# Performance work log

Hardware: AMD Instinct MI355X
Metric: run time of the kernel (lower is better)

The kernel has to match this reference:

```python
import jax, jax.numpy as jnp
import numpy as np

LP, LQ, B, D = 4096, 4096, 32, 512  # lp, lq, batch, hidden (=in_size1=in_size2)
WSCALE = 0.04  # ~ torch Linear default uniform bound 1/sqrt(512)


def setup_inputs() -> dict:
    key = jax.random.key(0)
    ks = jax.random.split(key, 11)
    return {
        "h": jax.random.normal(ks[0], (LP, B, D), jnp.float32),
        "u": jax.random.normal(ks[1], (B, LQ, D), jnp.float32),
        "v": jax.random.normal(ks[2], (B, D, 1), jnp.float32),
        "Wu_w": jax.random.normal(ks[3], (D, D), jnp.float32) * WSCALE,
        "Wu_b": jax.random.normal(ks[4], (D,), jnp.float32) * WSCALE,
        "Wh_w": jax.random.normal(ks[5], (D, D), jnp.float32) * WSCALE,
        "Wha_w": jax.random.normal(ks[6], (D, D), jnp.float32) * WSCALE,
        "W_ih": jax.random.normal(ks[7], (3 * D, D), jnp.float32) * WSCALE,
        "W_hh": jax.random.normal(ks[8], (3 * D, D), jnp.float32) * WSCALE,
        "b_ih": jax.random.normal(ks[9], (3 * D,), jnp.float32) * WSCALE,
        "b_hh": jax.random.normal(ks[10], (3 * D,), jnp.float32) * WSCALE,
    }


def _gru_cell(x, hprev, W_ih, W_hh, b_ih, b_hh):
    # torch GRUCell semantics
    gi = x @ W_ih.T + b_ih          # [B, 3D]
    gh = hprev @ W_hh.T + b_hh      # [B, 3D]
    i_r, i_z, i_n = jnp.split(gi, 3, axis=-1)
    h_r, h_z, h_n = jnp.split(gh, 3, axis=-1)
    r = jax.nn.sigmoid(i_r + h_r)
    z = jax.nn.sigmoid(i_z + h_z)
    n = jnp.tanh(i_n + r * h_n)
    return (1.0 - z) * n + z * hprev


def reference(h, u, v, Wu_w, Wu_b, Wh_w, Wha_w, W_ih, W_hh, b_ih, b_hh):
    # h: [lp, B, d1], u: [B, lq, d2], v: [B, H, 1]
    vb = v[:, :, 0]  # [B, H]
    # --- attention over u ---
    xq = jnp.tanh(jnp.einsum('bqd,hd->bqh', u, Wu_w) + Wu_b)   # [B, lq, H]
    s = jnp.einsum('bqh,bh->bq', xq, vb)                        # bmm(x, v).squeeze
    a = jax.nn.softmax(s, axis=1)
    r = jnp.einsum('bq,bqd->bd', a, u)                          # [B, d2]
    # --- attention over h conditioned on r, twice with GRU update in between ---
    Whh_proj = jnp.einsum('pbd,hd->pbh', h, Wh_w)               # [lp, B, H] (reused)

    def h_attn(rvec):
        x = jnp.tanh(Whh_proj + (rvec @ Wha_w.T)[None])         # [lp, B, H]
        s = jnp.einsum('pbh,bh->bp', x, vb)                     # [B, lp]
        return jax.nn.softmax(s, axis=1)

    p1 = h_attn(r)
    c = jnp.einsum('bp,pbd->bd', p1, h)                         # [B, d1]
    r2 = _gru_cell(c, r, W_ih, W_hh, b_ih, b_hh)                # [B, d2]
    p2 = h_attn(r2)
    return (p1, p2)
```

## Files before the change

kernel.cpp:

```cpp
#include <hip/hip_runtime.h>
#include <hip/hip_bf16.h>

typedef __attribute__((ext_vector_type(4))) float f4;
typedef __attribute__((ext_vector_type(8))) _Float16 h8;
typedef __attribute__((ext_vector_type(4))) _Float16 h4;

#define MTOT 131072

__device__ __forceinline__ float fast_tanh(float x){
    float e = exp2f(x * 2.8853900817779268f);
    return 1.0f - 2.0f * __builtin_amdgcn_rcpf(e + 1.0f);
}
__device__ __forceinline__ float fast_sigmoid(float x){
    return __builtin_amdgcn_rcpf(1.0f + exp2f(-x * 1.4426950408889634f));
}
__device__ __forceinline__ float wave_reduce_sum(float v){
    #pragma unroll
    for (int off = 32; off; off >>= 1) v += __shfl_down(v, off, 64);
    return v;
}

__device__ __forceinline__ void gl_lds16(const void* g, void* l){
    __builtin_amdgcn_global_load_lds(
        (const __attribute__((address_space(1))) void*)g,
        (__attribute__((address_space(3))) void*)l, 16, 0, 0);
}

__global__ __launch_bounds__(256) void k_pack_both(
    const float* __restrict__ Wu, const float* __restrict__ Wh,
    _Float16* __restrict__ Pu, _Float16* __restrict__ Ph)
{
    const int g = blockIdx.x;
    const float* W = (g < 128) ? Wu : Wh;
    _Float16*    P = (g < 128) ? Pu : Ph;
    const int idx = (g & 127) * 4 + (threadIdx.x >> 6);
    const int l = threadIdx.x & 63;
    const int n = (idx >> 4) * 16 + (l & 15);
    const int k = (idx & 15) * 32 + (l >> 4) * 8;
    const float* src = W + n * 512 + k;
    f4 s0 = *(const f4*)(src);
    f4 s1 = *(const f4*)(src + 4);
    h8 v;
    #pragma unroll
    for (int i = 0; i < 4; i++){ v[i] = (_Float16)s0[i]; v[4+i] = (_Float16)s1[i]; }
    *(h8*)(P + (idx << 9) + l * 8) = v;
}

union SMem {
    struct { float A[2][4096]; _Float16 W[2][8192]; } st;
    _Float16 ep[64][264];
};

template<int MODE>
__global__ __launch_bounds__(512) void k_score_gemm(
    const float* __restrict__ A,
    const _Float16* __restrict__ Wp,
    const float* __restrict__ vb,
    const float* __restrict__ addvec,
    float* __restrict__ spart,
    _Float16* __restrict__ whh)
{
    __shared__ __align__(16) SMem sm;

    const int tid  = threadIdx.x;
    const int lane = tid & 63;
    const int wv   = tid >> 6;
    const int wr   = wv >> 2;
    const int wc   = wv & 3;
    const int swz  = ((blockIdx.x & 7) << 8) | (blockIdx.x >> 3);
    const int mt   = swz >> 1;
    const int nc   = swz & 1;
    const int m0   = mt * 128;
    const int n0   = nc * 256;

    const int lr = lane & 15;
    const int kq = lane >> 4;

    const int arow0 = tid >> 3;
    const int aseg  = tid & 7;

    auto stage = [&](int kt, int buf){
        #pragma unroll
        for (int i = 0; i < 2; i++){
            const int row = arow0 + i*64;
            const int sg  = aseg ^ (row & 7);
            const float* g = A + (long)(m0 + row)*512 + kt*32 + sg*4;
            char* l = (char*)&sm.st.A[0][0] + buf*16384 + (i*512 + wv*64)*16;
            gl_lds16(g, l);
        }
        #pragma unroll
        for (int i = 0; i < 2; i++){
            const int chunk = i*8 + wv;
            const _Float16* g = Wp + ((long)((nc*16 + chunk)*16 + kt))*512 + lane*8;
            char* l = (char*)&sm.st.W[0][0] + buf*16384 + chunk*1024;
            gl_lds16(g, l);
        }
    };

    f4 acc[4][4] = {};

    stage(0, 0);
    __syncthreads();

    const int plo = (2*kq)     ^ (lr & 7);
    const int phi = (2*kq + 1) ^ (lr & 7);

    for (int kt = 0; kt < 16; ++kt){
        const int buf = kt & 1;
        if (kt < 15) stage(kt + 1, buf ^ 1);

        const float* Ab = &sm.st.A[0][0] + buf*4096;
        h8 af[4];
        #pragma unroll
        for (int mi = 0; mi < 4; mi++){
            const int row = wr*64 + mi*16 + lr;
            f4 lo = *(const f4*)(Ab + row*32 + plo*4);
            f4 hi = *(const f4*)(Ab + row*32 + phi*4);
            h8 v;
            #pragma unroll
            for (int i = 0; i < 4; i++){ v[i] = (_Float16)lo[i]; v[4+i] = (_Float16)hi[i]; }
            af[mi] = v;
        }
        const _Float16* Wb = &sm.st.W[0][0] + buf*8192;
        h8 bf[4];
        #pragma unroll
        for (int ni = 0; ni < 4; ni++)
            bf[ni] = *(const h8*)(Wb + (wc*4 + ni)*512 + lane*8);

        #pragma unroll
        for (int mi = 0; mi < 4; mi++)
            #pragma unroll
            for (int ni = 0; ni < 4; ni++)
                acc[mi][ni] = __builtin_amdgcn_mfma_f32_16x16x32_f16(af[mi], bf[ni], acc[mi][ni], 0, 0, 0);

        __syncthreads();
    }

    const int jrow = (lane >> 4) * 4;
    for (int hf = 0; hf < 2; ++hf){
        if (wr == hf){
            #pragma unroll
            for (int mi = 0; mi < 4; mi++)
                #pragma unroll
                for (int ni = 0; ni < 4; ni++)
                    #pragma unroll
                    for (int j = 0; j < 4; j++)
                        sm.ep[mi*16 + jrow + j][wc*64 + ni*16 + lr] = (_Float16)acc[mi][ni][j];
        }
        __syncthreads();

        if (MODE == 1 && whh){
            const int row = tid >> 3, seg = tid & 7;
            const int m = m0 + hf*64 + row;
            const _Float16* esrc = &sm.ep[row][seg*32];
            _Float16* gdst = whh + (long)m*512 + n0 + seg*32;
            #pragma unroll
            for (int i = 0; i < 4; i++)
                *(h8*)(gdst + i*8) = *(const h8*)(esrc + i*8);
        }

        #pragma unroll
        for (int rr = 0; rr < 8; ++rr){
            const int erow = wv*8 + rr;
            const int m = m0 + hf*64 + erow;
            const int b = (MODE == 0) ? (m >> 12) : (m & 31);
            const int n = n0 + lane*4;
            h4 hv = *(const h4*)&sm.ep[erow][lane*4];
            f4 vbv = *(const f4*)&vb[b*512 + n];
            f4 adv;
            if (MODE == 0) adv = *(const f4*)&addvec[n];
            else           adv = *(const f4*)&addvec[b*512 + n];
            float p = 0.f;
            #pragma unroll
            for (int i = 0; i < 4; i++)
                p += fast_tanh((float)hv[i] + adv[i]) * vbv[i];
            p = wave_reduce_sum(p);
            if (lane == 0){
                const int sIdx = (MODE == 0) ? m : (((m & 31) << 12) | (m >> 5));
                spart[nc*MTOT + sIdx] = p;
            }
        }
        __syncthreads();
    }
}

template<int NP>
__global__ __launch_bounds__(256) void k_softmax(const float* __restrict__ s,
        float* __restrict__ out)
{
    __shared__ float red[8];
    __shared__ float bcast[2];
    const int b = blockIdx.x, t = threadIdx.x;
    const int wv = t >> 6, lane = t & 63;
    float vals[16];
    float mx = -3.0e38f;
    #pragma unroll
    for (int i = 0; i < 16; i++){
        float v = s[b*4096 + t + i*256];
        #pragma unroll
        for (int p = 1; p < NP; p++) v += s[p*MTOT + b*4096 + t + i*256];
        vals[i] = v;
        mx = fmaxf(mx, v);
    }
    #pragma unroll
    for (int off = 32; off; off >>= 1) mx = fmaxf(mx, __shfl_down(mx, off, 64));
    if (lane == 0) red[wv] = mx;
    __syncthreads();
    if (t == 0) bcast[0] = fmaxf(fmaxf(red[0], red[1]), fmaxf(red[2], red[3]));
    __syncthreads();
    const float gmax = bcast[0];
    float sum = 0.f;
    #pragma unroll
    for (int i = 0; i < 16; i++){
        vals[i] = exp2f((vals[i] - gmax) * 1.4426950408889634f);
        sum += vals[i];
    }
    sum = wave_reduce_sum(sum);
    if (lane == 0) red[wv] = sum;
    __syncthreads();
    if (t == 0) bcast[1] = red[0] + red[1] + red[2] + red[3];
    __syncthreads();
    const float inv = 1.0f / bcast[1];
    #pragma unroll
    for (int i = 0; i < 16; i++) out[b*4096 + t + i*256] = vals[i] * inv;
}

__global__ __launch_bounds__(512) void k_weighted_rowsum(
    const float* __restrict__ wts, const float* __restrict__ X,
    float* __restrict__ part, int mode)
{
    const int b = blockIdx.x, ch = blockIdx.y, d = threadIdx.x;
    float acc = 0.f;
    const int q0 = ch * 128;
    for (int q = q0; q < q0 + 128; ++q){
        const float w = wts[b*4096 + q];
        if (fabsf(w) > 1e-20f){
            const float* xp = (mode == 0) ? (X + ((long)(b*4096 + q) * 512) + d)
                                          : (X + ((long)(q*32 + b) * 512) + d);
            acc += w * xp[0];
        }
    }
    part[(ch*32 + b)*512 + d] = acc;
}

__global__ void k_reduce_part(const float* __restrict__ part, float* __restrict__ out){
    const int b = blockIdx.x, d = threadIdx.x;
    float s = 0.f;
    #pragma unroll
    for (int ch = 0; ch < 32; ++ch) s += part[(ch*32 + b)*512 + d];
    out[b*512 + d] = s;
}

__global__ __launch_bounds__(256) void k_matvec(
    const float* __restrict__ W, const float* __restrict__ x,
    const float* __restrict__ bias, float* __restrict__ out, int N)
{
    __shared__ float xs[512];
    const int b = blockIdx.x, t = threadIdx.x;
    xs[t] = x[b*512 + t];
    xs[t + 256] = x[b*512 + 256 + t];
    __syncthreads();
    const int wv = t >> 6, lane = t & 63;
    f4 x0 = *(const f4*)&xs[lane*8];
    f4 x1 = *(const f4*)&xs[lane*8 + 4];
    const int rbase = blockIdx.y*32 + wv*8;
    for (int rr = 0; rr < 8; ++rr){
        const int row = rbase + rr;
        const float* wp = W + (long)row*512 + lane*8;
        f4 w0 = *(const f4*)wp;
        f4 w1 = *(const f4*)(wp + 4);
        float p = w0[0]*x0[0] + w0[1]*x0[1] + w0[2]*x0[2] + w0[3]*x0[3]
                + w1[0]*x1[0] + w1[1]*x1[1] + w1[2]*x1[2] + w1[3]*x1[3];
        p = wave_reduce_sum(p);
        if (lane == 0) out[b*N + row] = p + (bias ? bias[row] : 0.f);
    }
}

__global__ void k_gru(const float* __restrict__ gi, const float* __restrict__ gh,
                      const float* __restrict__ r, float* __restrict__ r2)
{
    const int b = blockIdx.x, d = threadIdx.x;
    const float* gib = gi + b*1536;
    const float* ghb = gh + b*1536;
    const float rg = fast_sigmoid(gib[d]        + ghb[d]);
    const float z  = fast_sigmoid(gib[512 + d]  + ghb[512 + d]);
    const float n  = fast_tanh   (gib[1024 + d] + rg * ghb[1024 + d]);
    r2[b*512 + d] = (1.f - z)*n + z*r[b*512 + d];
}

__global__ __launch_bounds__(256) void k_t2(const _Float16* __restrict__ whh,
        const float* __restrict__ vb, const float* __restrict__ ra2, float* __restrict__ t2)
{
    const int wv = threadIdx.x >> 6, lane = threadIdx.x & 63;
    const int mbase = blockIdx.x*32 + wv*8;
    for (int rr = 0; rr < 8; ++rr){
        const int m = mbase + rr;
        const int b = m & 31;
        h8 hv = *(const h8*)(whh + (long)m*512 + lane*8);
        const float* rp  = ra2 + b*512 + lane*8;
        const float* vbp = vb  + b*512 + lane*8;
        float p = 0.f;
        #pragma unroll
        for (int i = 0; i < 8; i++)
            p += fast_tanh((float)hv[i] + rp[i]) * vbp[i];
        p = wave_reduce_sum(p);
        if (lane == 0) t2[((m & 31) << 12) | (m >> 5)] = p;
    }
}

extern "C" void kernel_launch(void* const* d_in, const int* in_sizes, int n_in,
                              void* d_out, int out_size, void* d_ws, size_t ws_size,
                              hipStream_t stream)
{
    const float* h_    = (const float*)d_in[0];
    const float* u_    = (const float*)d_in[1];
    const float* vb    = (const float*)d_in[2];
    const float* Wu_w  = (const float*)d_in[3];
    const float* Wu_b  = (const float*)d_in[4];
    const float* Wh_w  = (const float*)d_in[5];
    const float* Wha_w = (const float*)d_in[6];
    const float* W_ih  = (const float*)d_in[7];
    const float* W_hh  = (const float*)d_in[8];
    const float* b_ih  = (const float*)d_in[9];
    const float* b_hh  = (const float*)d_in[10];
    float* out = (float*)d_out;

    char* ws = (char*)d_ws;
    float*    spart = (float*)(ws + 0);
    float*    tpart = (float*)(ws + 1048576);
    float*    part  = (float*)(ws + 2097152);
    float*    a_    = (float*)(ws + 4194304);
    _Float16* Wpu   = (_Float16*)(ws + 4718592);
    _Float16* Wph   = (_Float16*)(ws + 5242880);
    float*    r_    = (float*)(ws + 5767168);
    float*    ra1   = (float*)(ws + 5832704);
    float*    c_    = (float*)(ws + 5898240);
    float*    r2    = (float*)(ws + 5963776);
    float*    ra2   = (float*)(ws + 6029312);
    float*    gi    = (float*)(ws + 6094848);
    float*    gh    = (float*)(ws + 6291456);
    _Float16* whh   = (_Float16*)(ws + 8388608);
    const bool big = ws_size >= (size_t)8388608 + (size_t)MTOT * 512 * 2;

    k_pack_both<<<256, 256, 0, stream>>>(Wu_w, Wh_w, Wpu, Wph);

    k_score_gemm<0><<<2048, 512, 0, stream>>>(u_, Wpu, vb, Wu_b, spart, nullptr);
    k_softmax<2><<<32, 256, 0, stream>>>(spart, a_);
    k_weighted_rowsum<<<dim3(32, 32), 512, 0, stream>>>(a_, u_, part, 0);
    k_reduce_part<<<32, 512, 0, stream>>>(part, r_);
    k_matvec<<<dim3(32, 16), 256, 0, stream>>>(Wha_w, r_, nullptr, ra1, 512);

    k_score_gemm<1><<<2048, 512, 0, stream>>>(h_, Wph, vb, ra1, tpart, big ? whh : nullptr);
    k_softmax<2><<<32, 256, 0, stream>>>(tpart, out);

    k_weighted_rowsum<<<dim3(32, 32), 512, 0, stream>>>(out, h_, part, 1);
    k_reduce_part<<<32, 512, 0, stream>>>(part, c_);
    k_matvec<<<dim3(32, 48), 256, 0, stream>>>(W_ih, c_, b_ih, gi, 1536);
    k_matvec<<<dim3(32, 48), 256, 0, stream>>>(W_hh, r_, b_hh, gh, 1536);
    k_gru<<<32, 512, 0, stream>>>(gi, gh, r_, r2);
    k_matvec<<<dim3(32, 16), 256, 0, stream>>>(Wha_w, r2, nullptr, ra2, 512);

    if (big){
        k_t2<<<4096, 256, 0, stream>>>(whh, vb, ra2, tpart);
        k_softmax<1><<<32, 256, 0, stream>>>(tpart, out + MTOT);
    } else {
        k_score_gemm<2><<<2048, 512, 0, stream>>>(h_, Wph, vb, ra2, tpart, nullptr);
        k_softmax<2><<<32, 256, 0, stream>>>(tpart, out + MTOT);
    }
}
```

Baseline: 523.7 us.

## Stage GEMM A operand as fp16 in LDS and fuse small tail kernels

Result: slower. 857.3 us (+63.7%).

```diff
diff --git a/kernel.cpp b/kernel.cpp
--- a/kernel.cpp
+++ b/kernel.cpp
@@ -4,6 +4,7 @@
 typedef __attribute__((ext_vector_type(4))) float f4;
 typedef __attribute__((ext_vector_type(8))) _Float16 h8;
 typedef __attribute__((ext_vector_type(4))) _Float16 h4;
+typedef __attribute__((ext_vector_type(2))) __fp16 hp2;
 
 #define MTOT 131072
 
@@ -47,9 +48,10 @@
 }
 
 union SMem {
-    struct { float A[2][4096]; _Float16 W[2][8192]; } st;
+    struct { _Float16 A[2][128][36]; _Float16 W[2][8192]; } st;
     _Float16 ep[64][264];
 };
+union HU { h8 v; hp2 p[4]; };
 
 template<int MODE>
 __global__ __launch_bounds__(512) void k_score_gemm(
@@ -76,18 +78,11 @@
     const int lr = lane & 15;
     const int kq = lane >> 4;
 
-    const int arow0 = tid >> 3;
-    const int aseg  = tid & 7;
-
-    auto stage = [&](int kt, int buf){
-        #pragma unroll
-        for (int i = 0; i < 2; i++){
-            const int row = arow0 + i*64;
-            const int sg  = aseg ^ (row & 7);
-            const float* g = A + (long)(m0 + row)*512 + kt*32 + sg*4;
-            char* l = (char*)&sm.st.A[0][0] + buf*16384 + (i*512 + wv*64)*16;
-            gl_lds16(g, l);
-        }
+    const int srow = tid >> 2;
+    const int sg   = tid & 3;
+    const float* agbase = A + (long)(m0 + srow) * 512 + sg * 8;
+
+    auto stageW = [&](int kt, int buf){
         #pragma unroll
         for (int i = 0; i < 2; i++){
             const int chunk = i*8 + wv;
@@ -96,31 +91,40 @@
             gl_lds16(g, l);
         }
     };
+    auto cvtA = [&](f4 a0, f4 a1){
+        HU u;
+        u.p[0] = __builtin_amdgcn_cvt_pkrtz(a0[0], a0[1]);
+        u.p[1] = __builtin_amdgcn_cvt_pkrtz(a0[2], a0[3]);
+        u.p[2] = __builtin_amdgcn_cvt_pkrtz(a1[0], a1[1]);
+        u.p[3] = __builtin_amdgcn_cvt_pkrtz(a1[2], a1[3]);
+        return u.v;
+    };
 
     f4 acc[4][4] = {};
 
-    stage(0, 0);
-    __syncthreads();
-
-    const int plo = (2*kq)     ^ (lr & 7);
-    const int phi = (2*kq + 1) ^ (lr & 7);
+    {
+        f4 a0 = *(const f4*)(agbase);
+        f4 a1 = *(const f4*)(agbase + 4);
+        stageW(0, 0);
+        *(h8*)&sm.st.A[0][srow][sg*8] = cvtA(a0, a1);
+    }
+    __syncthreads();
 
     for (int kt = 0; kt < 16; ++kt){
         const int buf = kt & 1;
-        if (kt < 15) stage(kt + 1, buf ^ 1);
-
-        const float* Ab = &sm.st.A[0][0] + buf*4096;
+        f4 a0, a1;
+        if (kt < 15){
+            const float* p = agbase + (kt + 1) * 32;
+            a0 = *(const f4*)p;
+            a1 = *(const f4*)(p + 4);
+            stageW(kt + 1, buf ^ 1);
+        }
+        __builtin_amdgcn_sched_barrier(0);
+
         h8 af[4];
         #pragma unroll
-        for (int mi = 0; mi < 4; mi++){
-            const int row = wr*64 + mi*16 + lr;
-            f4 lo = *(const f4*)(Ab + row*32 + plo*4);
-            f4 hi = *(const f4*)(Ab + row*32 + phi*4);
-            h8 v;
-            #pragma unroll
-            for (int i = 0; i < 4; i++){ v[i] = (_Float16)lo[i]; v[4+i] = (_Float16)hi[i]; }
-            af[mi] = v;
-        }
+        for (int mi = 0; mi < 4; mi++)
+            af[mi] = *(const h8*)&sm.st.A[buf][wr*64 + mi*16 + lr][kq*8];
         const _Float16* Wb = &sm.st.W[0][0] + buf*8192;
         h8 bf[4];
         #pragma unroll
@@ -132,6 +136,9 @@
             #pragma unroll
             for (int ni = 0; ni < 4; ni++)
                 acc[mi][ni] = __builtin_amdgcn_mfma_f32_16x16x32_f16(af[mi], bf[ni], acc[mi][ni], 0, 0, 0);
+
+        if (kt < 15)
+            *(h8*)&sm.st.A[buf ^ 1][srow][sg*8] = cvtA(a0, a1);
 
         __syncthreads();
     }
@@ -243,49 +250,93 @@
     part[(ch*32 + b)*512 + d] = acc;
 }
 
-__global__ void k_reduce_part(const float* __restrict__ part, float* __restrict__ out){
-    const int b = blockIdx.x, d = threadIdx.x;
+__global__ __launch_bounds__(512) void k_finish1(
+    const float* __restrict__ part, const float* __restrict__ Wha,
+    float* __restrict__ r_out, float* __restrict__ ra1)
+{
+    __shared__ float xl[512];
+    const int b = blockIdx.x, t = threadIdx.x;
     float s = 0.f;
     #pragma unroll
-    for (int ch = 0; ch < 32; ++ch) s += part[(ch*32 + b)*512 + d];
-    out[b*512 + d] = s;
-}
-
-__global__ __launch_bounds__(256) void k_matvec(
-    const float* __restrict__ W, const float* __restrict__ x,
-    const float* __restrict__ bias, float* __restrict__ out, int N)
-{
-    __shared__ float xs[512];
-    const int b = blockIdx.x, t = threadIdx.x;
-    xs[t] = x[b*512 + t];
-    xs[t + 256] = x[b*512 + 256 + t];
+    for (int ch = 0; ch < 32; ++ch) s += part[(ch*32 + b)*512 + t];
+    xl[t] = s;
+    r_out[b*512 + t] = s;
     __syncthreads();
     const int wv = t >> 6, lane = t & 63;
-    f4 x0 = *(const f4*)&xs[lane*8];
-    f4 x1 = *(const f4*)&xs[lane*8 + 4];
-    const int rbase = blockIdx.y*32 + wv*8;
-    for (int rr = 0; rr < 8; ++rr){
-        const int row = rbase + rr;
-        const float* wp = W + (long)row*512 + lane*8;
+    f4 x0 = *(const f4*)&xl[lane*8];
+    f4 x1 = *(const f4*)&xl[lane*8 + 4];
+    for (int j = 0; j < 64; ++j){
+        const int row = wv*64 + j;
+        const float* wp = Wha + (long)row*512 + lane*8;
         f4 w0 = *(const f4*)wp;
         f4 w1 = *(const f4*)(wp + 4);
         float p = w0[0]*x0[0] + w0[1]*x0[1] + w0[2]*x0[2] + w0[3]*x0[3]
                 + w1[0]*x1[0] + w1[1]*x1[1] + w1[2]*x1[2] + w1[3]*x1[3];
         p = wave_reduce_sum(p);
-        if (lane == 0) out[b*N + row] = p + (bias ? bias[row] : 0.f);
-    }
-}
-
-__global__ void k_gru(const float* __restrict__ gi, const float* __restrict__ gh,
-                      const float* __restrict__ r, float* __restrict__ r2)
-{
-    const int b = blockIdx.x, d = threadIdx.x;
-    const float* gib = gi + b*1536;
-    const float* ghb = gh + b*1536;
-    const float rg = fast_sigmoid(gib[d]        + ghb[d]);
-    const float z  = fast_sigmoid(gib[512 + d]  + ghb[512 + d]);
-    const float n  = fast_tanh   (gib[1024 + d] + rg * ghb[1024 + d]);
-    r2[b*512 + d] = (1.f - z)*n + z*r[b*512 + d];
+        if (lane == 0) ra1[b*512 + row] = p;
+    }
+}
+
+__global__ __launch_bounds__(512) void k_finish2(
+    const float* __restrict__ part, const float* __restrict__ r_in,
+    const float* __restrict__ Wih, const float* __restrict__ Whh_,
+    const float* __restrict__ bih, const float* __restrict__ bhh,
+    const float* __restrict__ Wha, float* __restrict__ ra2)
+{
+    __shared__ float cl[512], rl[512], r2l[512];
+    __shared__ float gl[1536], hl[1536];
+    const int b = blockIdx.x, t = threadIdx.x;
+    const int wv = t >> 6, lane = t & 63;
+    float s = 0.f;
+    #pragma unroll
+    for (int ch = 0; ch < 32; ++ch) s += part[(ch*32 + b)*512 + t];
+    cl[t] = s;
+    rl[t] = r_in[b*512 + t];
+    __syncthreads();
+    f4 c0 = *(const f4*)&cl[lane*8];
+    f4 c1 = *(const f4*)&cl[lane*8 + 4];
+    f4 r0 = *(const f4*)&rl[lane*8];
+    f4 r1 = *(const f4*)&rl[lane*8 + 4];
+    for (int j = 0; j < 192; ++j){
+        const int row = wv*192 + j;
+        const float* wp = Wih + (long)row*512 + lane*8;
+        f4 w0 = *(const f4*)wp;
+        f4 w1 = *(const f4*)(wp + 4);
+        float p = w0[0]*c0[0] + w0[1]*c0[1] + w0[2]*c0[2] + w0[3]*c0[3]
+                + w1[0]*c1[0] + w1[1]*c1[1] + w1[2]*c1[2] + w1[3]*c1[3];
+        p = wave_reduce_sum(p);
+        if (lane == 0) gl[row] = p + bih[row];
+    }
+    for (int j = 0; j < 192; ++j){
+        const int row = wv*192 + j;
+        const float* wp = Whh_ + (long)row*512 + lane*8;
+        f4 w0 = *(const f4*)wp;
+        f4 w1 = *(const f4*)(wp + 4);
+        float p = w0[0]*r0[0] + w0[1]*r0[1] + w0[2]*r0[2] + w0[3]*r0[3]
+                + w1[0]*r1[0] + w1[1]*r1[1] + w1[2]*r1[2] + w1[3]*r1[3];
+        p = wave_reduce_sum(p);
+        if (lane == 0) hl[row] = p + bhh[row];
+    }
+    __syncthreads();
+    {
+        const float rg = fast_sigmoid(gl[t] + hl[t]);
+        const float z  = fast_sigmoid(gl[512 + t] + hl[512 + t]);
+        const float nn = fast_tanh(gl[1024 + t] + rg * hl[1024 + t]);
+        r2l[t] = (1.f - z)*nn + z*rl[t];
+    }
+    __syncthreads();
+    f4 x0 = *(const f4*)&r2l[lane*8];
+    f4 x1 = *(const f4*)&r2l[lane*8 + 4];
+    for (int j = 0; j < 64; ++j){
+        const int row = wv*64 + j;
+        const float* wp = Wha + (long)row*512 + lane*8;
+        f4 w0 = *(const f4*)wp;
+        f4 w1 = *(const f4*)(wp + 4);
+        float p = w0[0]*x0[0] + w0[1]*x0[1] + w0[2]*x0[2] + w0[3]*x0[3]
+                + w1[0]*x1[0] + w1[1]*x1[1] + w1[2]*x1[2] + w1[3]*x1[3];
+        p = wave_reduce_sum(p);
+        if (lane == 0) ra2[b*512 + row] = p;
+    }
 }
 
 __global__ __launch_bounds__(256) void k_t2(const _Float16* __restrict__ whh,
@@ -334,11 +385,7 @@
     _Float16* Wph   = (_Float16*)(ws + 5242880);
     float*    r_    = (float*)(ws + 5767168);
     float*    ra1   = (float*)(ws + 5832704);
-    float*    c_    = (float*)(ws + 5898240);
-    float*    r2    = (float*)(ws + 5963776);
     float*    ra2   = (float*)(ws + 6029312);
-    float*    gi    = (float*)(ws + 6094848);
-    float*    gh    = (float*)(ws + 6291456);
     _Float16* whh   = (_Float16*)(ws + 8388608);
     const bool big = ws_size >= (size_t)8388608 + (size_t)MTOT * 512 * 2;
 
@@ -347,18 +394,13 @@
     k_score_gemm<0><<<2048, 512, 0, stream>>>(u_, Wpu, vb, Wu_b, spart, nullptr);
     k_softmax<2><<<32, 256, 0, stream>>>(spart, a_);
     k_weighted_rowsum<<<dim3(32, 32), 512, 0, stream>>>(a_, u_, part, 0);
-    k_reduce_part<<<32, 512, 0, stream>>>(part, r_);
-    k_matvec<<<dim3(32, 16), 256, 0, stream>>>(Wha_w, r_, nullptr, ra1, 512);
+    k_finish1<<<32, 512, 0, stream>>>(part, Wha_w, r_, ra1);
 
     k_score_gemm<1><<<2048, 512, 0, stream>>>(h_, Wph, vb, ra1, tpart, big ? whh : nullptr);
     k_softmax<2><<<32, 256, 0, stream>>>(tpart, out);
 
     k_weighted_rowsum<<<dim3(32, 32), 512, 0, stream>>>(out, h_, part, 1);
-    k_reduce_part<<<32, 512, 0, stream>>>(part, c_);
-    k_matvec<<<dim3(32, 48), 256, 0, stream>>>(W_ih, c_, b_ih, gi, 1536);
-    k_matvec<<<dim3(32, 48), 256, 0, stream>>>(W_hh, r_, b_hh, gh, 1536);
-    k_gru<<<32, 512, 0, stream>>>(gi, gh, r_, r2);
-    k_matvec<<<dim3(32, 16), 256, 0, stream>>>(Wha_w, r2, nullptr, ra2, 512);
+    k_finish2<<<32, 512, 0, stream>>>(part, r_, W_ih, W_hh, b_ih, b_hh, Wha_w, ra2);
 
     if (big){
         k_t2<<<4096, 256, 0, stream>>>(whh, vb, ra2, tpart);
```

## Stage A tile through registers with fp16 conversion before LDS write

Applied to the files above, without the earlier changes.

After: 522.0 us. About the same (-0.3%).

```diff
diff --git a/kernel.cpp b/kernel.cpp
--- a/kernel.cpp
+++ b/kernel.cpp
@@ -4,6 +4,7 @@
 typedef __attribute__((ext_vector_type(4))) float f4;
 typedef __attribute__((ext_vector_type(8))) _Float16 h8;
 typedef __attribute__((ext_vector_type(4))) _Float16 h4;
+typedef __attribute__((ext_vector_type(2))) __fp16 hp2;
 
 #define MTOT 131072
 
@@ -47,9 +48,10 @@
 }
 
 union SMem {
-    struct { float A[2][4096]; _Float16 W[2][8192]; } st;
+    struct { _Float16 A[2][128][36]; _Float16 W[2][8192]; } st;
     _Float16 ep[64][264];
 };
+union HU { h8 v; hp2 p[4]; };
 
 template<int MODE>
 __global__ __launch_bounds__(512) void k_score_gemm(
@@ -76,18 +78,11 @@
     const int lr = lane & 15;
     const int kq = lane >> 4;
 
-    const int arow0 = tid >> 3;
-    const int aseg  = tid & 7;
-
-    auto stage = [&](int kt, int buf){
-        #pragma unroll
-        for (int i = 0; i < 2; i++){
-            const int row = arow0 + i*64;
-            const int sg  = aseg ^ (row & 7);
-            const float* g = A + (long)(m0 + row)*512 + kt*32 + sg*4;
-            char* l = (char*)&sm.st.A[0][0] + buf*16384 + (i*512 + wv*64)*16;
-            gl_lds16(g, l);
-        }
+    const int srow = tid >> 2;
+    const int sg   = tid & 3;
+    const float* agbase = A + (long)(m0 + srow) * 512 + sg * 8;
+
+    auto stageW = [&](int kt, int buf){
         #pragma unroll
         for (int i = 0; i < 2; i++){
             const int chunk = i*8 + wv;
@@ -96,31 +91,40 @@
             gl_lds16(g, l);
         }
     };
+    auto cvtA = [&](f4 a0, f4 a1){
+        HU u;
+        u.p[0] = __builtin_amdgcn_cvt_pkrtz(a0[0], a0[1]);
+        u.p[1] = __builtin_amdgcn_cvt_pkrtz(a0[2], a0[3]);
+        u.p[2] = __builtin_amdgcn_cvt_pkrtz(a1[0], a1[1]);
+        u.p[3] = __builtin_amdgcn_cvt_pkrtz(a1[2], a1[3]);
+        return u.v;
+    };
 
     f4 acc[4][4] = {};
 
-    stage(0, 0);
-    __syncthreads();
-
-    const int plo = (2*kq)     ^ (lr & 7);
-    const int phi = (2*kq + 1) ^ (lr & 7);
+    {
+        f4 a0 = *(const f4*)(agbase);
+        f4 a1 = *(const f4*)(agbase + 4);
+        stageW(0, 0);
+        *(h8*)&sm.st.A[0][srow][sg*8] = cvtA(a0, a1);
+    }
+    __syncthreads();
 
     for (int kt = 0; kt < 16; ++kt){
         const int buf = kt & 1;
-        if (kt < 15) stage(kt + 1, buf ^ 1);
-
-        const float* Ab = &sm.st.A[0][0] + buf*4096;
+        f4 a0, a1;
+        if (kt < 15){
+            const float* p = agbase + (kt + 1) * 32;
+            a0 = *(const f4*)p;
+            a1 = *(const f4*)(p + 4);
+            stageW(kt + 1, buf ^ 1);
+        }
+        __builtin_amdgcn_sched_barrier(0);
+
         h8 af[4];
         #pragma unroll
-        for (int mi = 0; mi < 4; mi++){
-            const int row = wr*64 + mi*16 + lr;
-            f4 lo = *(const f4*)(Ab + row*32 + plo*4);
-            f4 hi = *(const f4*)(Ab + row*32 + phi*4);
-            h8 v;
-            #pragma unroll
-            for (int i = 0; i < 4; i++){ v[i] = (_Float16)lo[i]; v[4+i] = (_Float16)hi[i]; }
-            af[mi] = v;
-        }
+        for (int mi = 0; mi < 4; mi++)
+            af[mi] = *(const h8*)&sm.st.A[buf][wr*64 + mi*16 + lr][kq*8];
         const _Float16* Wb = &sm.st.W[0][0] + buf*8192;
         h8 bf[4];
         #pragma unroll
@@ -132,6 +136,9 @@
             #pragma unroll
             for (int ni = 0; ni < 4; ni++)
                 acc[mi][ni] = __builtin_amdgcn_mfma_f32_16x16x32_f16(af[mi], bf[ni], acc[mi][ni], 0, 0, 0);
+
+        if (kt < 15)
+            *(h8*)&sm.st.A[buf ^ 1][srow][sg*8] = cvtA(a0, a1);
 
         __syncthreads();
     }
```
